# Performance work log

Measured on AMD Instinct MI355X. Metric: run time of the kernel, lower is better.

The kernel has to match this reference:

```python
import jax, jax.numpy as jnp
import numpy as np

B, C, H, W = 64, 1, 512, 512
THRESHOLD = 50.0
LEVELS = 3


def _haar_dwt2(x):
    """Single-level 2D Haar DWT on [B,H,W] (even H,W). Returns (cA,(cH,cV,cD)).
    Matches pywt 'haar' coefficient magnitudes (sign conventions are irrelevant
    to the loss, which is odd-symmetric through soft-threshold and uses |.|)."""
    a = x[:, 0::2, 0::2]
    b = x[:, 0::2, 1::2]
    c = x[:, 1::2, 0::2]
    d = x[:, 1::2, 1::2]
    half = jnp.float32(0.5)
    cA = (a + b + c + d) * half
    cH = (a + b - c - d) * half  # low along cols, high along rows
    cV = (a - b + c - d) * half  # high along cols, low along rows
    cD = (a - b - c + d) * half  # high/high
    return cA, (cH, cV, cD)


def _wavedec2(x, levels):
    """Multi-level DWT. Returns detail tuples ordered coarsest-first,
    matching pywt.wavedec2 list order coeffs[1:]."""
    details = []
    cA = x
    for _ in range(levels):
        cA, d = _haar_dwt2(cA)
        details.append(d)
    details.reverse()  # coarsest first
    return details


def _soft_threshold(x, thr):
    return jnp.sign(x) * jnp.maximum(jnp.abs(x) - thr, 0.0)


def setup_inputs() -> dict:
    key = jax.random.key(0)
    k1, k2 = jax.random.split(key)
    pred = jax.random.uniform(k1, (B, C, H, W), dtype=jnp.float32)
    target = jax.random.uniform(k2, (B, C, H, W), dtype=jnp.float32)
    return {"pred": pred, "target": target}


def reference(pred, target):
    p = pred[:, 0]   # [B,H,W]
    t = target[:, 0]
    det_p = _wavedec2(p, LEVELS)
    det_t = _wavedec2(t, LEVELS)
    total = jnp.float32(0.0)
    for level_idx in range(1, LEVELS + 1):
        # per-level adaptive threshold, normalized to [0,1] image range
        thr = jnp.float32((THRESHOLD / 2.0 ** (level_idx - 1)) / 255.0)
        level_weight = jnp.float32(1.0 / level_idx)
        dp = det_p[level_idx - 1]
        dt = det_t[level_idx - 1]
        level_loss = jnp.float32(0.0)
        for k in range(3):  # cH, cV, cD
            diff = _soft_threshold(dp[k], thr) - _soft_threshold(dt[k], thr)
            level_loss = level_loss + jnp.mean(jnp.abs(diff))
        total = total + level_weight * level_loss / 3.0
    # per-sample sum / valid_samples == batch mean (all samples valid here)
    return total
```

## Files before the change

kernel.cpp:

```cpp
#include <hip/hip_runtime.h>


#define IMG_H 512
#define IMG_W 512
#define N_BATCH 64

#define THR1 (50.0f / 255.0f)
#define THR2 (25.0f / 255.0f)
#define THR3 (12.5f / 255.0f)

__device__ __forceinline__ float softthr(float x, float thr) {
    float m = fmaxf(fabsf(x) - thr, 0.0f);
    return copysignf(m, x);
}

__device__ __forceinline__ float detail_term(float p, float t, float thr) {
    return fabsf(softthr(p, thr) - softthr(t, thr));
}

__device__ __forceinline__ void haar_quad(float a, float b, float c, float d,
                                          float& cA, float& cH, float& cV, float& cD) {
    cA = 0.5f * (a + b + c + d);
    cH = 0.5f * (a + b - c - d);
    cV = 0.5f * (a - b + c - d);
    cD = 0.5f * (a - b - c + d);
}

__global__ void zero_out_kernel(float* out) { out[0] = 0.0f; }

__global__ __launch_bounds__(256)
void wavelet_loss_kernel(const float* __restrict__ pred,
                         const float* __restrict__ target,
                         float* __restrict__ out) {
    const int tid  = blockIdx.x * 256 + threadIdx.x;
    const int img  = tid >> 14;
    const int rem  = tid & 16383;
    const int w    = rem >> 6;
    const int lane = rem & 63;
    const int wy   = w >> 2;
    const int wx   = w & 3;
    const int q    = lane >> 2;
    const int sub  = lane & 3;
    const int dy   = sub >> 1;
    const int dx   = sub & 1;

    const int r2 = wy * 2 + dy;
    const int c2 = wx * 32 + q * 2 + dx;

    const long base = (long)img * (IMG_H * IMG_W) + (long)(r2 * 4) * IMG_W + c2 * 4;

    float4 p0 = *(const float4*)(pred + base);
    float4 p1 = *(const float4*)(pred + base + IMG_W);
    float4 p2 = *(const float4*)(pred + base + 2 * IMG_W);
    float4 p3 = *(const float4*)(pred + base + 3 * IMG_W);
    float4 t0 = *(const float4*)(target + base);
    float4 t1 = *(const float4*)(target + base + IMG_W);
    float4 t2 = *(const float4*)(target + base + 2 * IMG_W);
    float4 t3 = *(const float4*)(target + base + 3 * IMG_W);

    float s1 = 0.0f;
    float cA1p[4], cA1t[4];

    {
        float cA, cH, cV, cD, cAt_, cHt, cVt, cDt;
        haar_quad(p0.x, p0.y, p1.x, p1.y, cA, cH, cV, cD);
        haar_quad(t0.x, t0.y, t1.x, t1.y, cAt_, cHt, cVt, cDt);
        s1 += detail_term(cH, cHt, THR1) + detail_term(cV, cVt, THR1) + detail_term(cD, cDt, THR1);
        cA1p[0] = cA; cA1t[0] = cAt_;
        haar_quad(p0.z, p0.w, p1.z, p1.w, cA, cH, cV, cD);
        haar_quad(t0.z, t0.w, t1.z, t1.w, cAt_, cHt, cVt, cDt);
        s1 += detail_term(cH, cHt, THR1) + detail_term(cV, cVt, THR1) + detail_term(cD, cDt, THR1);
        cA1p[1] = cA; cA1t[1] = cAt_;
        haar_quad(p2.x, p2.y, p3.x, p3.y, cA, cH, cV, cD);
        haar_quad(t2.x, t2.y, t3.x, t3.y, cAt_, cHt, cVt, cDt);
        s1 += detail_term(cH, cHt, THR1) + detail_term(cV, cVt, THR1) + detail_term(cD, cDt, THR1);
        cA1p[2] = cA; cA1t[2] = cAt_;
        haar_quad(p2.z, p2.w, p3.z, p3.w, cA, cH, cV, cD);
        haar_quad(t2.z, t2.w, t3.z, t3.w, cAt_, cHt, cVt, cDt);
        s1 += detail_term(cH, cHt, THR1) + detail_term(cV, cVt, THR1) + detail_term(cD, cDt, THR1);
        cA1p[3] = cA; cA1t[3] = cAt_;
    }

    float s2 = 0.0f;
    float cA2p, cA2t;
    {
        float cH, cV, cD, cHt, cVt, cDt;
        haar_quad(cA1p[0], cA1p[1], cA1p[2], cA1p[3], cA2p, cH, cV, cD);
        haar_quad(cA1t[0], cA1t[1], cA1t[2], cA1t[3], cA2t, cHt, cVt, cDt);
        s2 += detail_term(cH, cHt, THR2) + detail_term(cV, cVt, THR2) + detail_term(cD, cDt, THR2);
    }

    float s3 = 0.0f;
    {
        float vp[4], vt[4];
        vp[sub]     = cA2p;               vt[sub]     = cA2t;
        vp[sub ^ 1] = __shfl_xor(cA2p, 1); vt[sub ^ 1] = __shfl_xor(cA2t, 1);
        vp[sub ^ 2] = __shfl_xor(cA2p, 2); vt[sub ^ 2] = __shfl_xor(cA2t, 2);
        vp[sub ^ 3] = __shfl_xor(cA2p, 3); vt[sub ^ 3] = __shfl_xor(cA2t, 3);
        float cA, cH, cV, cD, cAt_, cHt, cVt, cDt;
        haar_quad(vp[0], vp[1], vp[2], vp[3], cA, cH, cV, cD);
        haar_quad(vt[0], vt[1], vt[2], vt[3], cAt_, cHt, cVt, cDt);
        s3 = detail_term(cH, cHt, THR3) + detail_term(cV, cVt, THR3) + detail_term(cD, cDt, THR3);
    }

    constexpr float W1 = 1.0f / (1.0f * 3.0f * (float)(N_BATCH * 256 * 256));
    constexpr float W2 = 1.0f / (2.0f * 3.0f * (float)(N_BATCH * 128 * 128));
    constexpr float W3 = 1.0f / (3.0f * 3.0f * (float)(N_BATCH * 64 * 64));

    float v = W1 * s1 + W2 * s2;
    v += (sub == 0 ? W3 : 0.0f) * s3;

    #pragma unroll
    for (int off = 32; off > 0; off >>= 1)
        v += __shfl_down(v, off, 64);

    __shared__ float wave_sums[4];
    const int lane_b = threadIdx.x & 63;
    const int wave_b = threadIdx.x >> 6;
    if (lane_b == 0) wave_sums[wave_b] = v;
    __syncthreads();
    if (threadIdx.x == 0) {
        float s = wave_sums[0] + wave_sums[1] + wave_sums[2] + wave_sums[3];
        atomicAdd(out, s);
    }
}

extern "C" void kernel_launch(void* const* d_in, const int* in_sizes, int n_in,
                              void* d_out, int out_size, void* d_ws, size_t ws_size,
                              hipStream_t stream) {
    const float* pred   = (const float*)d_in[0];
    const float* target = (const float*)d_in[1];
    float* out = (float*)d_out;

    zero_out_kernel<<<1, 1, 0, stream>>>(out);

    wavelet_loss_kernel<<<4096, 256, 0, stream>>>(pred, target, out);
}
```

Before: 164.9 us.

## Remap thread layout for coalesced rows, two tiles per thread, two-pass reduction

Changes the thread-to-pixel mapping so each half-wave reads a contiguous 512-byte row span instead of scattered 2x2 quad blocks, which makes the global loads better coalesced. The level-3 neighbours are now gathered with xor-32 and xor-1 shuffles. The grid is halved, with each thread processing two tiles, and the per-block atomicAdd plus zero-init kernel are replaced by per-block partial sums in workspace followed by a single-block reduce kernel. This adds a dependency on workspace size and gives fewer resident blocks to hide memory latency.

```diff
diff --git a/kernel.cpp b/kernel.cpp
--- a/kernel.cpp
+++ b/kernel.cpp
@@ -8,6 +8,9 @@
 #define THR1 (50.0f / 255.0f)
 #define THR2 (25.0f / 255.0f)
 #define THR3 (12.5f / 255.0f)
+
+#define GRID_BLOCKS 2048
+#define N_ITERS 2
 
 __device__ __forceinline__ float softthr(float x, float thr) {
     float m = fmaxf(fabsf(x) - thr, 0.0f);
@@ -26,103 +29,126 @@
     cD = 0.5f * (a - b - c + d);
 }
 
-__global__ void zero_out_kernel(float* out) { out[0] = 0.0f; }
-
-__global__ __launch_bounds__(256)
-void wavelet_loss_kernel(const float* __restrict__ pred,
-                         const float* __restrict__ target,
-                         float* __restrict__ out) {
-    const int tid  = blockIdx.x * 256 + threadIdx.x;
-    const int img  = tid >> 14;
-    const int rem  = tid & 16383;
-    const int w    = rem >> 6;
-    const int lane = rem & 63;
-    const int wy   = w >> 2;
-    const int wx   = w & 3;
-    const int q    = lane >> 2;
-    const int sub  = lane & 3;
-    const int dy   = sub >> 1;
-    const int dx   = sub & 1;
-
-    const int r2 = wy * 2 + dy;
-    const int c2 = wx * 32 + q * 2 + dx;
-
-    const long base = (long)img * (IMG_H * IMG_W) + (long)(r2 * 4) * IMG_W + c2 * 4;
-
-    float4 p0 = *(const float4*)(pred + base);
-    float4 p1 = *(const float4*)(pred + base + IMG_W);
-    float4 p2 = *(const float4*)(pred + base + 2 * IMG_W);
-    float4 p3 = *(const float4*)(pred + base + 3 * IMG_W);
-    float4 t0 = *(const float4*)(target + base);
-    float4 t1 = *(const float4*)(target + base + IMG_W);
-    float4 t2 = *(const float4*)(target + base + 2 * IMG_W);
-    float4 t3 = *(const float4*)(target + base + 3 * IMG_W);
-
-    float s1 = 0.0f;
-    float cA1p[4], cA1t[4];
-
-    {
-        float cA, cH, cV, cD, cAt_, cHt, cVt, cDt;
-        haar_quad(p0.x, p0.y, p1.x, p1.y, cA, cH, cV, cD);
-        haar_quad(t0.x, t0.y, t1.x, t1.y, cAt_, cHt, cVt, cDt);
-        s1 += detail_term(cH, cHt, THR1) + detail_term(cV, cVt, THR1) + detail_term(cD, cDt, THR1);
-        cA1p[0] = cA; cA1t[0] = cAt_;
-        haar_quad(p0.z, p0.w, p1.z, p1.w, cA, cH, cV, cD);
-        haar_quad(t0.z, t0.w, t1.z, t1.w, cAt_, cHt, cVt, cDt);
-        s1 += detail_term(cH, cHt, THR1) + detail_term(cV, cVt, THR1) + detail_term(cD, cDt, THR1);
-        cA1p[1] = cA; cA1t[1] = cAt_;
-        haar_quad(p2.x, p2.y, p3.x, p3.y, cA, cH, cV, cD);
-        haar_quad(t2.x, t2.y, t3.x, t3.y, cAt_, cHt, cVt, cDt);
-        s1 += detail_term(cH, cHt, THR1) + detail_term(cV, cVt, THR1) + detail_term(cD, cDt, THR1);
-        cA1p[2] = cA; cA1t[2] = cAt_;
-        haar_quad(p2.z, p2.w, p3.z, p3.w, cA, cH, cV, cD);
-        haar_quad(t2.z, t2.w, t3.z, t3.w, cAt_, cHt, cVt, cDt);
-        s1 += detail_term(cH, cHt, THR1) + detail_term(cV, cVt, THR1) + detail_term(cD, cDt, THR1);
-        cA1p[3] = cA; cA1t[3] = cAt_;
-    }
-
-    float s2 = 0.0f;
-    float cA2p, cA2t;
-    {
-        float cH, cV, cD, cHt, cVt, cDt;
-        haar_quad(cA1p[0], cA1p[1], cA1p[2], cA1p[3], cA2p, cH, cV, cD);
-        haar_quad(cA1t[0], cA1t[1], cA1t[2], cA1t[3], cA2t, cHt, cVt, cDt);
-        s2 += detail_term(cH, cHt, THR2) + detail_term(cV, cVt, THR2) + detail_term(cD, cDt, THR2);
-    }
-
-    float s3 = 0.0f;
-    {
-        float vp[4], vt[4];
-        vp[sub]     = cA2p;               vt[sub]     = cA2t;
-        vp[sub ^ 1] = __shfl_xor(cA2p, 1); vt[sub ^ 1] = __shfl_xor(cA2t, 1);
-        vp[sub ^ 2] = __shfl_xor(cA2p, 2); vt[sub ^ 2] = __shfl_xor(cA2t, 2);
-        vp[sub ^ 3] = __shfl_xor(cA2p, 3); vt[sub ^ 3] = __shfl_xor(cA2t, 3);
-        float cA, cH, cV, cD, cAt_, cHt, cVt, cDt;
-        haar_quad(vp[0], vp[1], vp[2], vp[3], cA, cH, cV, cD);
-        haar_quad(vt[0], vt[1], vt[2], vt[3], cAt_, cHt, cVt, cDt);
-        s3 = detail_term(cH, cHt, THR3) + detail_term(cV, cVt, THR3) + detail_term(cD, cDt, THR3);
-    }
-
+__global__ __launch_bounds__(256, 8)
+void wavelet_main(const float* __restrict__ pred,
+                  const float* __restrict__ target,
+                  float* __restrict__ ws) {
     constexpr float W1 = 1.0f / (1.0f * 3.0f * (float)(N_BATCH * 256 * 256));
     constexpr float W2 = 1.0f / (2.0f * 3.0f * (float)(N_BATCH * 128 * 128));
     constexpr float W3 = 1.0f / (3.0f * 3.0f * (float)(N_BATCH * 64 * 64));
 
-    float v = W1 * s1 + W2 * s2;
-    v += (sub == 0 ? W3 : 0.0f) * s3;
+    const int tid0 = blockIdx.x * 256 + threadIdx.x;
+    float acc = 0.0f;
+
+    #pragma unroll
+    for (int iter = 0; iter < N_ITERS; ++iter) {
+        const int it   = tid0 + iter * (GRID_BLOCKS * 256);
+        const int lane = it & 63;
+        const int wv   = it >> 6;
+        const int img  = wv >> 8;
+        const int ww   = wv & 255;
+        const int wcy  = ww >> 2;
+        const int wcx  = ww & 3;
+        const int half = lane >> 5;
+        const int li   = lane & 31;
+
+        const int r0 = 8 * wcy + 4 * half;
+        const int c0 = 128 * wcx + 4 * li;
+        const long base = (long)img * (IMG_H * IMG_W) + (long)r0 * IMG_W + c0;
+
+        const float4 p0 = *(const float4*)(pred + base);
+        const float4 p1 = *(const float4*)(pred + base + IMG_W);
+        const float4 p2 = *(const float4*)(pred + base + 2 * IMG_W);
+        const float4 p3 = *(const float4*)(pred + base + 3 * IMG_W);
+        const float4 t0 = *(const float4*)(target + base);
+        const float4 t1 = *(const float4*)(target + base + IMG_W);
+        const float4 t2 = *(const float4*)(target + base + 2 * IMG_W);
+        const float4 t3 = *(const float4*)(target + base + 3 * IMG_W);
+
+        float s1 = 0.0f;
+        float cA1p[4], cA1t[4];
+        {
+            float cA, cH, cV, cD, cAt, cHt, cVt, cDt;
+            haar_quad(p0.x, p0.y, p1.x, p1.y, cA, cH, cV, cD);
+            haar_quad(t0.x, t0.y, t1.x, t1.y, cAt, cHt, cVt, cDt);
+            s1 += detail_term(cH, cHt, THR1) + detail_term(cV, cVt, THR1) + detail_term(cD, cDt, THR1);
+            cA1p[0] = cA; cA1t[0] = cAt;
+
+            haar_quad(p0.z, p0.w, p1.z, p1.w, cA, cH, cV, cD);
+            haar_quad(t0.z, t0.w, t1.z, t1.w, cAt, cHt, cVt, cDt);
+            s1 += detail_term(cH, cHt, THR1) + detail_term(cV, cVt, THR1) + detail_term(cD, cDt, THR1);
+            cA1p[1] = cA; cA1t[1] = cAt;
+
+            haar_quad(p2.x, p2.y, p3.x, p3.y, cA, cH, cV, cD);
+            haar_quad(t2.x, t2.y, t3.x, t3.y, cAt, cHt, cVt, cDt);
+            s1 += detail_term(cH, cHt, THR1) + detail_term(cV, cVt, THR1) + detail_term(cD, cDt, THR1);
+            cA1p[2] = cA; cA1t[2] = cAt;
+
+            haar_quad(p2.z, p2.w, p3.z, p3.w, cA, cH, cV, cD);
+            haar_quad(t2.z, t2.w, t3.z, t3.w, cAt, cHt, cVt, cDt);
+            s1 += detail_term(cH, cHt, THR1) + detail_term(cV, cVt, THR1) + detail_term(cD, cDt, THR1);
+            cA1p[3] = cA; cA1t[3] = cAt;
+        }
+
+        float s2 = 0.0f;
+        float cA2p, cA2t;
+        {
+            float cH, cV, cD, cHt, cVt, cDt;
+            haar_quad(cA1p[0], cA1p[1], cA1p[2], cA1p[3], cA2p, cH, cV, cD);
+            haar_quad(cA1t[0], cA1t[1], cA1t[2], cA1t[3], cA2t, cHt, cVt, cDt);
+            s2 = detail_term(cH, cHt, THR2) + detail_term(cV, cVt, THR2) + detail_term(cD, cDt, THR2);
+        }
+
+        float s3 = 0.0f;
+        {
+            float pV = __shfl_xor(cA2p, 32);
+            float tV = __shfl_xor(cA2t, 32);
+            float pH = __shfl_xor(cA2p, 1);
+            float tH = __shfl_xor(cA2t, 1);
+            float pD = __shfl_xor(pV, 1);
+            float tD = __shfl_xor(tV, 1);
+            float cA, cH, cV, cD, cAt, cHt, cVt, cDt;
+            haar_quad(cA2p, pH, pV, pD, cA, cH, cV, cD);
+            haar_quad(cA2t, tH, tV, tD, cAt, cHt, cVt, cDt);
+            s3 = detail_term(cH, cHt, THR3) + detail_term(cV, cVt, THR3) + detail_term(cD, cDt, THR3);
+        }
+        const float w3 = ((lane & 33) == 0) ? W3 : 0.0f;
+
+        acc += W1 * s1 + W2 * s2 + w3 * s3;
+    }
+
+    #pragma unroll
+    for (int off = 32; off > 0; off >>= 1)
+        acc += __shfl_down(acc, off, 64);
+
+    __shared__ float wave_sums[4];
+    const int lane_b = threadIdx.x & 63;
+    const int wave_b = threadIdx.x >> 6;
+    if (lane_b == 0) wave_sums[wave_b] = acc;
+    __syncthreads();
+    if (threadIdx.x == 0)
+        ws[blockIdx.x] = wave_sums[0] + wave_sums[1] + wave_sums[2] + wave_sums[3];
+}
+
+__global__ __launch_bounds__(256)
+void wavelet_reduce(const float* __restrict__ ws, float* __restrict__ out) {
+    const int tidx = threadIdx.x;
+    float v = 0.0f;
+    #pragma unroll
+    for (int k = 0; k < GRID_BLOCKS / 256; ++k)
+        v += ws[tidx + k * 256];
 
     #pragma unroll
     for (int off = 32; off > 0; off >>= 1)
         v += __shfl_down(v, off, 64);
 
     __shared__ float wave_sums[4];
-    const int lane_b = threadIdx.x & 63;
-    const int wave_b = threadIdx.x >> 6;
-    if (lane_b == 0) wave_sums[wave_b] = v;
+    const int lane = tidx & 63;
+    const int wave = tidx >> 6;
+    if (lane == 0) wave_sums[wave] = v;
     __syncthreads();
-    if (threadIdx.x == 0) {
-        float s = wave_sums[0] + wave_sums[1] + wave_sums[2] + wave_sums[3];
-        atomicAdd(out, s);
-    }
+    if (tidx == 0)
+        out[0] = wave_sums[0] + wave_sums[1] + wave_sums[2] + wave_sums[3];
 }
 
 extern "C" void kernel_launch(void* const* d_in, const int* in_sizes, int n_in,
@@ -131,8 +157,8 @@
     const float* pred   = (const float*)d_in[0];
     const float* target = (const float*)d_in[1];
     float* out = (float*)d_out;
+    float* ws  = (float*)d_ws;
 
-    zero_out_kernel<<<1, 1, 0, stream>>>(out);
-
-    wavelet_loss_kernel<<<4096, 256, 0, stream>>>(pred, target, out);
+    wavelet_main<<<GRID_BLOCKS, 256, 0, stream>>>(pred, target, ws);
+    wavelet_reduce<<<1, 256, 0, stream>>>(ws, out);
 }
```

Result: faster. 141.4 us (-14.3%).
